# Kernel optimization log

Measured on AMD Instinct MI355X. Metric: run time of the kernel, lower is better.

Reference implementation:

```python
import jax, jax.numpy as jnp
import numpy as np

N_NODES = 10000
N_EDGES = 640000
N_GRAPHS = 64
IN_FEATS = 128
H_FEATS = 128


def setup_inputs() -> dict:
    key = jax.random.key(0)
    ks = jax.random.split(key, 8)
    in_feat = jax.random.normal(ks[0], (N_NODES, IN_FEATS), dtype=jnp.float32)
    src = jax.random.randint(ks[1], (N_EDGES,), 0, N_NODES, dtype=jnp.int32)
    dst = jax.random.randint(ks[2], (N_EDGES,), 0, N_NODES, dtype=jnp.int32)
    graph_ids = jnp.sort(jax.random.randint(ks[3], (N_NODES,), 0, N_GRAPHS, dtype=jnp.int32))
    s1 = 1.0 / np.sqrt(IN_FEATS)
    s2 = 1.0 / np.sqrt(H_FEATS)
    W1 = jax.random.uniform(ks[4], (IN_FEATS, H_FEATS), jnp.float32, -s1, s1)
    b1 = jnp.zeros((H_FEATS,), jnp.float32)
    W2 = jax.random.uniform(ks[5], (H_FEATS, H_FEATS), jnp.float32, -s2, s2)
    b2 = jnp.zeros((H_FEATS,), jnp.float32)
    Wd = jax.random.uniform(ks[6], (H_FEATS, 1), jnp.float32, -s2, s2)
    bd = jnp.zeros((1,), jnp.float32)
    return {"in_feat": in_feat, "src": src, "dst": dst, "graph_ids": graph_ids,
            "W1": W1, "b1": b1, "W2": W2, "b2": b2, "Wd": Wd, "bd": bd}


def _graph_conv(x, src, dst, norm_src, norm_dst, W, b):
    # DGL GraphConv, norm='both': D_dst^{-1/2} A D_src^{-1/2} X W + b
    x = x * norm_src[:, None]
    agg = jax.ops.segment_sum(x[src], dst, num_segments=N_NODES)  # scatter-add over edges
    agg = agg * norm_dst[:, None]
    return agg @ W + b


def reference(in_feat, src, dst, graph_ids, W1, b1, W2, b2, Wd, bd):
    ones_e = jnp.ones((N_EDGES,), in_feat.dtype)
    out_deg = jax.ops.segment_sum(ones_e, src, num_segments=N_NODES)
    in_deg = jax.ops.segment_sum(ones_e, dst, num_segments=N_NODES)
    norm_src = jnp.where(out_deg > 0, out_deg, 1.0) ** -0.5
    norm_dst = jnp.where(in_deg > 0, in_deg, 1.0) ** -0.5

    h = jax.nn.relu(_graph_conv(in_feat, src, dst, norm_src, norm_dst, W1, b1))
    h = jax.nn.relu(_graph_conv(h, src, dst, norm_src, norm_dst, W2, b2))

    # dgl.mean_nodes: per-graph mean of node features
    counts = jax.ops.segment_sum(jnp.ones((N_NODES,), h.dtype), graph_ids, num_segments=N_GRAPHS)
    pooled = jax.ops.segment_sum(h, graph_ids, num_segments=N_GRAPHS)
    pooled = pooled / jnp.maximum(counts, 1.0)[:, None]

    out = pooled @ Wd + bd  # [G, 1]
    return out.squeeze(-1)
```

## Files before the change

kernel.cpp:

```cpp
#include <hip/hip_runtime.h>
#include <hip/hip_fp16.h>

#define N_NODES 10000
#define N_EDGES 640000
#define N_GRAPHS 64
#define FEATS 128
#define CAP 128
#define NSLICE 128
#define EPS (N_EDGES / NSLICE)
#define EB (N_EDGES / 1024)
#define DSTRIDE 4
#define NTILE (N_NODES / 16)

static inline size_t align_up(size_t x, size_t a) { return (x + a - 1) & ~(a - 1); }

__global__ __launch_bounds__(256) void init_kernel(int* __restrict__ gcur,
                                                   int* __restrict__ deg_out,
                                                   float* __restrict__ graph_sum) {
    int i = blockIdx.x * 256 + threadIdx.x;
    if (i < N_NODES) gcur[i] = i * CAP;
    if (i < N_NODES * DSTRIDE) deg_out[i] = 0;
    if (i < N_GRAPHS) graph_sum[i] = 0.f;
}

__global__ __launch_bounds__(256) void scatter_deg_kernel(const int* __restrict__ src,
                                                          const int* __restrict__ dst,
                                                          int* __restrict__ gcur,
                                                          int* __restrict__ deg_out,
                                                          int* __restrict__ sorted_src) {
    const int tid = threadIdx.x;
    if (blockIdx.x < NSLICE) {
        __shared__ int cnt[N_NODES];
        const int s = blockIdx.x;
        for (int i = tid; i < N_NODES; i += 256) cnt[i] = 0;
        __syncthreads();
        const int4* d4 = (const int4*)(dst + s * EPS);
        for (int i = tid; i < EPS / 4; i += 256) {
            int4 dv = d4[i];
            atomicAdd(&cnt[dv.x], 1);
            atomicAdd(&cnt[dv.y], 1);
            atomicAdd(&cnt[dv.z], 1);
            atomicAdd(&cnt[dv.w], 1);
        }
        __syncthreads();
        for (int n = tid; n < N_NODES; n += 256) {
            int c = cnt[n];
            if (c) cnt[n] = atomicAdd(&gcur[n], c);
        }
        __syncthreads();
        const int4* s4 = (const int4*)(src + s * EPS);
        for (int i = tid; i < EPS / 4; i += 256) {
            int4 sv = s4[i];
            int4 dv = d4[i];
            int p;
            p = atomicAdd(&cnt[dv.x], 1); sorted_src[p] = sv.x;
            p = atomicAdd(&cnt[dv.y], 1); sorted_src[p] = sv.y;
            p = atomicAdd(&cnt[dv.z], 1); sorted_src[p] = sv.z;
            p = atomicAdd(&cnt[dv.w], 1); sorted_src[p] = sv.w;
        }
    } else {
        const int i = (blockIdx.x - NSLICE) * 256 + tid;
        int4 sv = ((const int4*)src)[i];
        atomicAdd(&deg_out[sv.x * DSTRIDE], 1);
        atomicAdd(&deg_out[sv.y * DSTRIDE], 1);
        atomicAdd(&deg_out[sv.z * DSTRIDE], 1);
        atomicAdd(&deg_out[sv.w * DSTRIDE], 1);
    }
}

__global__ __launch_bounds__(256) void prescale_kernel(const float* __restrict__ in_feat,
                                                       const int* __restrict__ deg_out,
                                                       __half* __restrict__ xs) {
    int i = blockIdx.x * 256 + threadIdx.x;
    if (i < N_NODES * (FEATS / 4)) {
        int n = i >> 5;
        int d = deg_out[n * DSTRIDE];
        float s = rsqrtf((float)(d < 1 ? 1 : d));
        float4 v = ((const float4*)in_feat)[i];
        __half2* o = (__half2*)(xs + (size_t)i * 4);
        o[0] = __floats2half2_rn(v.x * s, v.y * s);
        o[1] = __floats2half2_rn(v.z * s, v.w * s);
    }
}

static __device__ __forceinline__ void acc_row(uint4 v, float* a) {
    const __half2* hp = (const __half2*)&v;
#pragma unroll
    for (int j = 0; j < 4; j++) {
        float2 f = __half22float2(hp[j]);
        a[2 * j]     += f.x;
        a[2 * j + 1] += f.y;
    }
}

static __device__ __forceinline__ void qg_aggregate(const __half* __restrict__ X,
                                                    const int* __restrict__ ss,
                                                    int n, int cnt, int l16, float nd,
                                                    float* __restrict__ Arow) {
    const uint4* __restrict__ x4 = (const uint4*)X;
    const int base = n * CAP;
    float a[8] = {0.f, 0.f, 0.f, 0.f, 0.f, 0.f, 0.f, 0.f};
    int c = 0;
    for (; c + 8 <= cnt; c += 8) {
        int4 i0 = *(const int4*)(ss + base + c);
        int4 i1 = *(const int4*)(ss + base + c + 4);
        uint4 v0 = x4[i0.x * 16 + l16];
        uint4 v1 = x4[i0.y * 16 + l16];
        uint4 v2 = x4[i0.z * 16 + l16];
        uint4 v3 = x4[i0.w * 16 + l16];
        uint4 v4 = x4[i1.x * 16 + l16];
        uint4 v5 = x4[i1.y * 16 + l16];
        uint4 v6 = x4[i1.z * 16 + l16];
        uint4 v7 = x4[i1.w * 16 + l16];
        acc_row(v0, a); acc_row(v1, a); acc_row(v2, a); acc_row(v3, a);
        acc_row(v4, a); acc_row(v5, a); acc_row(v6, a); acc_row(v7, a);
    }
    for (; c < cnt; c++) acc_row(x4[ss[base + c] * 16 + l16], a);
    *(float4*)(Arow + l16 * 8)     = make_float4(a[0] * nd, a[1] * nd, a[2] * nd, a[3] * nd);
    *(float4*)(Arow + l16 * 8 + 4) = make_float4(a[4] * nd, a[5] * nd, a[6] * nd, a[7] * nd);
}

static __device__ __forceinline__ void gemm_2x4(const float* __restrict__ a0p,
                                                const float* __restrict__ a1p,
                                                const float* __restrict__ W, int fg,
                                                float4& acc0, float4& acc1) {
#pragma unroll 4
    for (int k = 0; k < FEATS; k++) {
        float a0 = a0p[k];
        float a1 = a1p[k];
        float4 w = *(const float4*)(W + k * FEATS + fg);
        acc0.x = fmaf(a0, w.x, acc0.x); acc0.y = fmaf(a0, w.y, acc0.y);
        acc0.z = fmaf(a0, w.z, acc0.z); acc0.w = fmaf(a0, w.w, acc0.w);
        acc1.x = fmaf(a1, w.x, acc1.x); acc1.y = fmaf(a1, w.y, acc1.y);
        acc1.z = fmaf(a1, w.z, acc1.z); acc1.w = fmaf(a1, w.w, acc1.w);
    }
}

__global__ __launch_bounds__(256) void fused_layer1_kernel(const __half* __restrict__ xs,
                                                           const int* __restrict__ sorted_src,
                                                           const int* __restrict__ gcur,
                                                           const int* __restrict__ deg_out,
                                                           const float* __restrict__ W,
                                                           const float* __restrict__ bias,
                                                           __half* __restrict__ out) {
    __shared__ float As[16 * FEATS];
    const int tid = threadIdx.x;
    const int nb = blockIdx.x * 16;
    const int lane = tid & 63;
    const int ln = (tid >> 6) * 4 + (lane >> 4);
    const int l16 = lane & 15;
    const int n = nb + ln;
    const int cnt = gcur[n] - n * CAP;
    const float nd = rsqrtf((float)(cnt < 1 ? 1 : cnt));
    qg_aggregate(xs, sorted_src, n, cnt, l16, nd, As + ln * FEATS);
    __syncthreads();
    const int fg = (tid & 31) << 2;
    const int r = tid >> 5;
    float4 acc0 = make_float4(0.f, 0.f, 0.f, 0.f);
    float4 acc1 = make_float4(0.f, 0.f, 0.f, 0.f);
    gemm_2x4(As + r * FEATS, As + (r + 8) * FEATS, W, fg, acc0, acc1);
    float4 bb = *(const float4*)(bias + fg);
    const int gn0 = nb + r, gn1 = nb + r + 8;
    const int do0 = deg_out[gn0 * DSTRIDE], do1 = deg_out[gn1 * DSTRIDE];
    const float s0 = rsqrtf((float)(do0 < 1 ? 1 : do0));
    const float s1 = rsqrtf((float)(do1 < 1 ? 1 : do1));
    __half2 h00 = __floats2half2_rn(fmaxf(acc0.x + bb.x, 0.f) * s0,
                                    fmaxf(acc0.y + bb.y, 0.f) * s0);
    __half2 h01 = __floats2half2_rn(fmaxf(acc0.z + bb.z, 0.f) * s0,
                                    fmaxf(acc0.w + bb.w, 0.f) * s0);
    __half2 h10 = __floats2half2_rn(fmaxf(acc1.x + bb.x, 0.f) * s1,
                                    fmaxf(acc1.y + bb.y, 0.f) * s1);
    __half2 h11 = __floats2half2_rn(fmaxf(acc1.z + bb.z, 0.f) * s1,
                                    fmaxf(acc1.w + bb.w, 0.f) * s1);
    __half2* o0 = (__half2*)(out + (size_t)gn0 * FEATS + fg);
    __half2* o1 = (__half2*)(out + (size_t)gn1 * FEATS + fg);
    o0[0] = h00; o0[1] = h01;
    o1[0] = h10; o1[1] = h11;
}

__global__ __launch_bounds__(256) void fused_layer2_kernel(const __half* __restrict__ hbuf,
                                                           const int* __restrict__ sorted_src,
                                                           const int* __restrict__ gcur,
                                                           const float* __restrict__ W,
                                                           const float* __restrict__ bias,
                                                           const float* __restrict__ Wd,
                                                           const int* __restrict__ gids,
                                                           float* __restrict__ graph_sum) {
    __shared__ float As[16 * FEATS];
    __shared__ float bins[N_GRAPHS];
    const int tid = threadIdx.x;
    const int nb = blockIdx.x * 16;
    const int lane = tid & 63;
    const int ln = (tid >> 6) * 4 + (lane >> 4);
    const int l16 = lane & 15;
    if (tid < N_GRAPHS) bins[tid] = 0.f;
    const int n = nb + ln;
    const int cnt = gcur[n] - n * CAP;
    const float nd = rsqrtf((float)(cnt < 1 ? 1 : cnt));
    qg_aggregate(hbuf, sorted_src, n, cnt, l16, nd, As + ln * FEATS);
    __syncthreads();
    const int fg = (tid & 31) << 2;
    const int r = tid >> 5;
    float4 acc0 = make_float4(0.f, 0.f, 0.f, 0.f);
    float4 acc1 = make_float4(0.f, 0.f, 0.f, 0.f);
    gemm_2x4(As + r * FEATS, As + (r + 8) * FEATS, W, fg, acc0, acc1);
    float4 bb = *(const float4*)(bias + fg);
    float4 wd = *(const float4*)(Wd + fg);
    float p0 = fmaxf(acc0.x + bb.x, 0.f) * wd.x + fmaxf(acc0.y + bb.y, 0.f) * wd.y +
               fmaxf(acc0.z + bb.z, 0.f) * wd.z + fmaxf(acc0.w + bb.w, 0.f) * wd.w;
    float p1 = fmaxf(acc1.x + bb.x, 0.f) * wd.x + fmaxf(acc1.y + bb.y, 0.f) * wd.y +
               fmaxf(acc1.z + bb.z, 0.f) * wd.z + fmaxf(acc1.w + bb.w, 0.f) * wd.w;
#pragma unroll
    for (int d = 16; d >= 1; d >>= 1) {
        p0 += __shfl_down(p0, d);
        p1 += __shfl_down(p1, d);
    }
    if ((tid & 31) == 0) {
        atomicAdd(&bins[gids[nb + r]], p0);
        atomicAdd(&bins[gids[nb + r + 8]], p1);
    }
    __syncthreads();
    if (tid < N_GRAPHS) {
        float v = bins[tid];
        if (v != 0.f) atomicAdd(&graph_sum[tid], v);
    }
}

static __device__ __forceinline__ int lower_bound_dev(const int* __restrict__ g, int key) {
    int lo = 0, hi = N_NODES;
    while (lo < hi) {
        int mid = (lo + hi) >> 1;
        if (g[mid] < key) lo = mid + 1; else hi = mid;
    }
    return lo;
}

__global__ __launch_bounds__(64) void final_kernel(const float* __restrict__ graph_sum,
                                                   const int* __restrict__ gids,
                                                   const float* __restrict__ bd,
                                                   float* __restrict__ out) {
    int g = threadIdx.x;
    if (g < N_GRAPHS) {
        int cnt = lower_bound_dev(gids, g + 1) - lower_bound_dev(gids, g);
        out[g] = graph_sum[g] / fmaxf((float)cnt, 1.f) + bd[0];
    }
}

extern "C" void kernel_launch(void* const* d_in, const int* in_sizes, int n_in,
                              void* d_out, int out_size, void* d_ws, size_t ws_size,
                              hipStream_t stream) {
    const float* in_feat = (const float*)d_in[0];
    const int*   src     = (const int*)d_in[1];
    const int*   dst     = (const int*)d_in[2];
    const int*   gids    = (const int*)d_in[3];
    const float* W1      = (const float*)d_in[4];
    const float* b1      = (const float*)d_in[5];
    const float* W2      = (const float*)d_in[6];
    const float* b2      = (const float*)d_in[7];
    const float* Wd      = (const float*)d_in[8];
    const float* bd      = (const float*)d_in[9];
    float* out = (float*)d_out;

    char* ws = (char*)d_ws;
    size_t off = 0;
    int* gcur = (int*)(ws + off);    off += (size_t)N_NODES * 4;
    off = align_up(off, 512);
    int* deg_out = (int*)(ws + off); off += (size_t)N_NODES * DSTRIDE * 4;
    off = align_up(off, 512);
    float* graph_sum = (float*)(ws + off); off += N_GRAPHS * 4;
    off = align_up(off, 512);
    int* sorted_src = (int*)(ws + off); off += (size_t)N_NODES * CAP * 4;
    off = align_up(off, 512);
    __half* xs = (__half*)(ws + off); off += (size_t)N_NODES * FEATS * 2;
    off = align_up(off, 512);
    __half* h  = (__half*)(ws + off); off += (size_t)N_NODES * FEATS * 2;
    (void)ws_size;

    init_kernel<<<(N_NODES * DSTRIDE + 255) / 256, 256, 0, stream>>>(gcur, deg_out, graph_sum);

    scatter_deg_kernel<<<NSLICE + EB, 256, 0, stream>>>(src, dst, gcur, deg_out, sorted_src);

    prescale_kernel<<<(N_NODES * (FEATS / 4) + 255) / 256, 256, 0, stream>>>(in_feat, deg_out, xs);

    fused_layer1_kernel<<<NTILE, 256, 0, stream>>>(xs, sorted_src, gcur, deg_out,
                                                   W1, b1, h);
    fused_layer2_kernel<<<NTILE, 256, 0, stream>>>(h, sorted_src, gcur,
                                                   W2, b2, Wd, gids, graph_sum);
    final_kernel<<<1, 64, 0, stream>>>(graph_sum, gids, bd, out);
}
```

Baseline: 184.4 us.

## Build CSR via two-pass bucketed sort with 16-bit indices and shared-memory tiles

Replaces the per-slice full-node shared histogram scatter with a two-level bucket sort. Edges are first binned into 128-node buckets through a shared staging area, then each bucket is sorted into a shared-memory CSR tile of 16-bit source indices and written out coalesced. Prescaling is fused into the same launch, and the gather loop is unrolled to 16 loads. The aim is to cut the scattered global atomics and the 10000-entry shared histogram clears, and to halve index traffic. In exchange it adds a staging buffer, assumes bucket capacity and at most 128 in-edges per node (truncating silently), and needs node ids to fit in 14 bits.

```diff
diff --git a/kernel.cpp b/kernel.cpp
--- a/kernel.cpp
+++ b/kernel.cpp
@@ -6,80 +6,132 @@
 #define N_GRAPHS 64
 #define FEATS 128
 #define CAP 128
-#define NSLICE 128
-#define EPS (N_EDGES / NSLICE)
-#define EB (N_EDGES / 1024)
+#define NB 79
+#define BCAP 12288
+#define ABLK 157
 #define DSTRIDE 4
 #define NTILE (N_NODES / 16)
+#define PRE_BLOCKS 1250
 
 static inline size_t align_up(size_t x, size_t a) { return (x + a - 1) & ~(a - 1); }
 
-__global__ __launch_bounds__(256) void init_kernel(int* __restrict__ gcur,
-                                                   int* __restrict__ deg_out,
-                                                   float* __restrict__ graph_sum) {
+__global__ __launch_bounds__(256) void zero_kernel(int* __restrict__ p, int n) {
     int i = blockIdx.x * 256 + threadIdx.x;
-    if (i < N_NODES) gcur[i] = i * CAP;
-    if (i < N_NODES * DSTRIDE) deg_out[i] = 0;
-    if (i < N_GRAPHS) graph_sum[i] = 0.f;
-}
-
-__global__ __launch_bounds__(256) void scatter_deg_kernel(const int* __restrict__ src,
-                                                          const int* __restrict__ dst,
-                                                          int* __restrict__ gcur,
-                                                          int* __restrict__ deg_out,
-                                                          int* __restrict__ sorted_src) {
+    if (i < n) p[i] = 0;
+}
+
+__global__ __launch_bounds__(256) void bucket_kernel(const int* __restrict__ src,
+                                                     const int* __restrict__ dst,
+                                                     int* __restrict__ bucket_cur,
+                                                     int* __restrict__ deg_out,
+                                                     int* __restrict__ staging) {
     const int tid = threadIdx.x;
-    if (blockIdx.x < NSLICE) {
-        __shared__ int cnt[N_NODES];
-        const int s = blockIdx.x;
-        for (int i = tid; i < N_NODES; i += 256) cnt[i] = 0;
-        __syncthreads();
-        const int4* d4 = (const int4*)(dst + s * EPS);
-        for (int i = tid; i < EPS / 4; i += 256) {
-            int4 dv = d4[i];
-            atomicAdd(&cnt[dv.x], 1);
-            atomicAdd(&cnt[dv.y], 1);
-            atomicAdd(&cnt[dv.z], 1);
-            atomicAdd(&cnt[dv.w], 1);
-        }
-        __syncthreads();
-        for (int n = tid; n < N_NODES; n += 256) {
-            int c = cnt[n];
-            if (c) cnt[n] = atomicAdd(&gcur[n], c);
-        }
-        __syncthreads();
-        const int4* s4 = (const int4*)(src + s * EPS);
-        for (int i = tid; i < EPS / 4; i += 256) {
-            int4 sv = s4[i];
-            int4 dv = d4[i];
+    if (blockIdx.x < ABLK) {
+        __shared__ int stage[4096];
+        __shared__ int hist[NB], pfx[NB], gbase[NB], cur[NB];
+        if (tid < NB) hist[tid] = 0;
+        __syncthreads();
+        int4 sv[4], dv[4];
+        bool valid[4];
+        const int base4 = blockIdx.x * 1024 + tid;
+#pragma unroll
+        for (int k = 0; k < 4; k++) {
+            int i4 = base4 + k * 256;
+            valid[k] = (i4 < N_EDGES / 4);
+            sv[k] = make_int4(0, 0, 0, 0);
+            dv[k] = make_int4(0, 0, 0, 0);
+            if (valid[k]) { sv[k] = ((const int4*)src)[i4]; dv[k] = ((const int4*)dst)[i4]; }
+        }
+#pragma unroll
+        for (int k = 0; k < 4; k++) if (valid[k]) {
+            atomicAdd(&hist[dv[k].x >> 7], 1);
+            atomicAdd(&hist[dv[k].y >> 7], 1);
+            atomicAdd(&hist[dv[k].z >> 7], 1);
+            atomicAdd(&hist[dv[k].w >> 7], 1);
+        }
+        __syncthreads();
+        if (tid == 0) {
+            int run = 0;
+            for (int b = 0; b < NB; b++) { pfx[b] = run; run += hist[b]; }
+        }
+        __syncthreads();
+        if (tid < NB) {
+            int c = hist[tid];
+            gbase[tid] = c ? atomicAdd(&bucket_cur[tid], c) : 0;
+            cur[tid] = pfx[tid];
+        }
+        __syncthreads();
+#pragma unroll
+        for (int k = 0; k < 4; k++) if (valid[k]) {
             int p;
-            p = atomicAdd(&cnt[dv.x], 1); sorted_src[p] = sv.x;
-            p = atomicAdd(&cnt[dv.y], 1); sorted_src[p] = sv.y;
-            p = atomicAdd(&cnt[dv.z], 1); sorted_src[p] = sv.z;
-            p = atomicAdd(&cnt[dv.w], 1); sorted_src[p] = sv.w;
+            p = atomicAdd(&cur[dv[k].x >> 7], 1); stage[p] = (sv[k].x << 14) | dv[k].x;
+            p = atomicAdd(&cur[dv[k].y >> 7], 1); stage[p] = (sv[k].y << 14) | dv[k].y;
+            p = atomicAdd(&cur[dv[k].z >> 7], 1); stage[p] = (sv[k].z << 14) | dv[k].z;
+            p = atomicAdd(&cur[dv[k].w >> 7], 1); stage[p] = (sv[k].w << 14) | dv[k].w;
+        }
+        __syncthreads();
+        const int wv = tid >> 6, ln = tid & 63;
+        for (int b = wv; b < NB; b += 4) {
+            const int c = hist[b], gb = gbase[b], lb = pfx[b];
+            for (int k = ln; k < c; k += 64) staging[b * BCAP + gb + k] = stage[lb + k];
         }
     } else {
-        const int i = (blockIdx.x - NSLICE) * 256 + tid;
-        int4 sv = ((const int4*)src)[i];
-        atomicAdd(&deg_out[sv.x * DSTRIDE], 1);
-        atomicAdd(&deg_out[sv.y * DSTRIDE], 1);
-        atomicAdd(&deg_out[sv.z * DSTRIDE], 1);
-        atomicAdd(&deg_out[sv.w * DSTRIDE], 1);
-    }
-}
-
-__global__ __launch_bounds__(256) void prescale_kernel(const float* __restrict__ in_feat,
-                                                       const int* __restrict__ deg_out,
-                                                       __half* __restrict__ xs) {
-    int i = blockIdx.x * 256 + threadIdx.x;
-    if (i < N_NODES * (FEATS / 4)) {
-        int n = i >> 5;
-        int d = deg_out[n * DSTRIDE];
-        float s = rsqrtf((float)(d < 1 ? 1 : d));
-        float4 v = ((const float4*)in_feat)[i];
-        __half2* o = (__half2*)(xs + (size_t)i * 4);
-        o[0] = __floats2half2_rn(v.x * s, v.y * s);
-        o[1] = __floats2half2_rn(v.z * s, v.w * s);
+        const int base4 = (blockIdx.x - ABLK) * 1024 + tid;
+#pragma unroll
+        for (int k = 0; k < 4; k++) {
+            int i4 = base4 + k * 256;
+            if (i4 < N_EDGES / 4) {
+                int4 s = ((const int4*)src)[i4];
+                atomicAdd(&deg_out[s.x * DSTRIDE], 1);
+                atomicAdd(&deg_out[s.y * DSTRIDE], 1);
+                atomicAdd(&deg_out[s.z * DSTRIDE], 1);
+                atomicAdd(&deg_out[s.w * DSTRIDE], 1);
+            }
+        }
+    }
+}
+
+__global__ __launch_bounds__(256) void csr_prescale_kernel(const int* __restrict__ bucket_cur,
+                                                           const int* __restrict__ staging,
+                                                           unsigned short* __restrict__ csr,
+                                                           int* __restrict__ deg_in,
+                                                           const int* __restrict__ deg_out,
+                                                           const float* __restrict__ in_feat,
+                                                           __half* __restrict__ xs) {
+    const int tid = threadIdx.x;
+    if (blockIdx.x < NB) {
+        __shared__ unsigned short tile[128 * CAP];
+        __shared__ int cur[128];
+        const int b = blockIdx.x;
+        if (tid < 128) cur[tid] = 0;
+        __syncthreads();
+        const int cnt = bucket_cur[b];
+        const int* st = staging + b * BCAP;
+        for (int i = tid; i < cnt; i += 256) {
+            int e = st[i];
+            int dl = (e & 16383) - b * 128;
+            int p = atomicAdd(&cur[dl], 1);
+            if (p < CAP) tile[dl * CAP + p] = (unsigned short)(e >> 14);
+        }
+        __syncthreads();
+        const uint4* t4 = (const uint4*)tile;
+        uint4* c4 = (uint4*)(csr + (size_t)b * 128 * CAP);
+        for (int i = tid; i < 128 * CAP / 8; i += 256) c4[i] = t4[i];
+        if (tid < 128) {
+            int n = b * 128 + tid;
+            if (n < N_NODES) deg_in[n] = cur[tid] < CAP ? cur[tid] : CAP;
+        }
+    } else {
+        int i = (blockIdx.x - NB) * 256 + tid;
+        if (i < N_NODES * (FEATS / 4)) {
+            int n = i >> 5;
+            int d = deg_out[n * DSTRIDE];
+            float s = rsqrtf((float)(d < 1 ? 1 : d));
+            float4 v = ((const float4*)in_feat)[i];
+            __half2* o = (__half2*)(xs + (size_t)i * 4);
+            o[0] = __floats2half2_rn(v.x * s, v.y * s);
+            o[1] = __floats2half2_rn(v.z * s, v.w * s);
+        }
     }
 }
 
@@ -94,28 +146,37 @@
 }
 
 static __device__ __forceinline__ void qg_aggregate(const __half* __restrict__ X,
-                                                    const int* __restrict__ ss,
+                                                    const unsigned short* __restrict__ csr,
                                                     int n, int cnt, int l16, float nd,
                                                     float* __restrict__ Arow) {
     const uint4* __restrict__ x4 = (const uint4*)X;
-    const int base = n * CAP;
+    const unsigned short* __restrict__ ss = csr + (size_t)n * CAP;
     float a[8] = {0.f, 0.f, 0.f, 0.f, 0.f, 0.f, 0.f, 0.f};
     int c = 0;
-    for (; c + 8 <= cnt; c += 8) {
-        int4 i0 = *(const int4*)(ss + base + c);
-        int4 i1 = *(const int4*)(ss + base + c + 4);
-        uint4 v0 = x4[i0.x * 16 + l16];
-        uint4 v1 = x4[i0.y * 16 + l16];
-        uint4 v2 = x4[i0.z * 16 + l16];
-        uint4 v3 = x4[i0.w * 16 + l16];
-        uint4 v4 = x4[i1.x * 16 + l16];
-        uint4 v5 = x4[i1.y * 16 + l16];
-        uint4 v6 = x4[i1.z * 16 + l16];
-        uint4 v7 = x4[i1.w * 16 + l16];
-        acc_row(v0, a); acc_row(v1, a); acc_row(v2, a); acc_row(v3, a);
-        acc_row(v4, a); acc_row(v5, a); acc_row(v6, a); acc_row(v7, a);
-    }
-    for (; c < cnt; c++) acc_row(x4[ss[base + c] * 16 + l16], a);
+    for (; c + 16 <= cnt; c += 16) {
+        uint4 iv0 = *(const uint4*)(ss + c);
+        uint4 iv1 = *(const uint4*)(ss + c + 8);
+        const unsigned short* i0 = (const unsigned short*)&iv0;
+        const unsigned short* i1 = (const unsigned short*)&iv1;
+        uint4 v[16];
+#pragma unroll
+        for (int k = 0; k < 8; k++) v[k] = x4[(int)i0[k] * 16 + l16];
+#pragma unroll
+        for (int k = 0; k < 8; k++) v[8 + k] = x4[(int)i1[k] * 16 + l16];
+#pragma unroll
+        for (int k = 0; k < 16; k++) acc_row(v[k], a);
+    }
+    if (c + 8 <= cnt) {
+        uint4 iv0 = *(const uint4*)(ss + c);
+        const unsigned short* i0 = (const unsigned short*)&iv0;
+        uint4 v[8];
+#pragma unroll
+        for (int k = 0; k < 8; k++) v[k] = x4[(int)i0[k] * 16 + l16];
+#pragma unroll
+        for (int k = 0; k < 8; k++) acc_row(v[k], a);
+        c += 8;
+    }
+    for (; c < cnt; c++) acc_row(x4[(int)ss[c] * 16 + l16], a);
     *(float4*)(Arow + l16 * 8)     = make_float4(a[0] * nd, a[1] * nd, a[2] * nd, a[3] * nd);
     *(float4*)(Arow + l16 * 8 + 4) = make_float4(a[4] * nd, a[5] * nd, a[6] * nd, a[7] * nd);
 }
@@ -137,8 +198,8 @@
 }
 
 __global__ __launch_bounds__(256) void fused_layer1_kernel(const __half* __restrict__ xs,
-                                                           const int* __restrict__ sorted_src,
-                                                           const int* __restrict__ gcur,
+                                                           const unsigned short* __restrict__ csr,
+                                                           const int* __restrict__ deg_in,
                                                            const int* __restrict__ deg_out,
                                                            const float* __restrict__ W,
                                                            const float* __restrict__ bias,
@@ -150,9 +211,9 @@
     const int ln = (tid >> 6) * 4 + (lane >> 4);
     const int l16 = lane & 15;
     const int n = nb + ln;
-    const int cnt = gcur[n] - n * CAP;
+    const int cnt = deg_in[n];
     const float nd = rsqrtf((float)(cnt < 1 ? 1 : cnt));
-    qg_aggregate(xs, sorted_src, n, cnt, l16, nd, As + ln * FEATS);
+    qg_aggregate(xs, csr, n, cnt, l16, nd, As + ln * FEATS);
     __syncthreads();
     const int fg = (tid & 31) << 2;
     const int r = tid >> 5;
@@ -179,8 +240,8 @@
 }
 
 __global__ __launch_bounds__(256) void fused_layer2_kernel(const __half* __restrict__ hbuf,
-                                                           const int* __restrict__ sorted_src,
-                                                           const int* __restrict__ gcur,
+                                                           const unsigned short* __restrict__ csr,
+                                                           const int* __restrict__ deg_in,
                                                            const float* __restrict__ W,
                                                            const float* __restrict__ bias,
                                                            const float* __restrict__ Wd,
@@ -195,9 +256,9 @@
     const int l16 = lane & 15;
     if (tid < N_GRAPHS) bins[tid] = 0.f;
     const int n = nb + ln;
-    const int cnt = gcur[n] - n * CAP;
+    const int cnt = deg_in[n];
     const float nd = rsqrtf((float)(cnt < 1 ? 1 : cnt));
-    qg_aggregate(hbuf, sorted_src, n, cnt, l16, nd, As + ln * FEATS);
+    qg_aggregate(hbuf, csr, n, cnt, l16, nd, As + ln * FEATS);
     __syncthreads();
     const int fg = (tid & 31) << 2;
     const int r = tid >> 5;
@@ -263,28 +324,31 @@
 
     char* ws = (char*)d_ws;
     size_t off = 0;
-    int* gcur = (int*)(ws + off);    off += (size_t)N_NODES * 4;
-    off = align_up(off, 512);
-    int* deg_out = (int*)(ws + off); off += (size_t)N_NODES * DSTRIDE * 4;
-    off = align_up(off, 512);
+    int* bucket_cur = (int*)(ws + off); off += NB * 4;
+    int* deg_out = (int*)(ws + off);    off += (size_t)N_NODES * DSTRIDE * 4;
     float* graph_sum = (float*)(ws + off); off += N_GRAPHS * 4;
-    off = align_up(off, 512);
-    int* sorted_src = (int*)(ws + off); off += (size_t)N_NODES * CAP * 4;
+    const int zero_n = (int)(off / 4);
+    off = align_up(off, 512);
+    int* deg_in = (int*)(ws + off);  off += (size_t)N_NODES * 4;
+    off = align_up(off, 512);
+    int* staging = (int*)(ws + off); off += (size_t)NB * BCAP * 4;
+    off = align_up(off, 512);
+    unsigned short* csr = (unsigned short*)(ws + off);
+    off += (size_t)NB * 128 * CAP * 2;
     off = align_up(off, 512);
     __half* xs = (__half*)(ws + off); off += (size_t)N_NODES * FEATS * 2;
     off = align_up(off, 512);
     __half* h  = (__half*)(ws + off); off += (size_t)N_NODES * FEATS * 2;
     (void)ws_size;
 
-    init_kernel<<<(N_NODES * DSTRIDE + 255) / 256, 256, 0, stream>>>(gcur, deg_out, graph_sum);
-
-    scatter_deg_kernel<<<NSLICE + EB, 256, 0, stream>>>(src, dst, gcur, deg_out, sorted_src);
-
-    prescale_kernel<<<(N_NODES * (FEATS / 4) + 255) / 256, 256, 0, stream>>>(in_feat, deg_out, xs);
-
-    fused_layer1_kernel<<<NTILE, 256, 0, stream>>>(xs, sorted_src, gcur, deg_out,
-                                                   W1, b1, h);
-    fused_layer2_kernel<<<NTILE, 256, 0, stream>>>(h, sorted_src, gcur,
-                                                   W2, b2, Wd, gids, graph_sum);
+    zero_kernel<<<(zero_n + 255) / 256, 256, 0, stream>>>((int*)ws, zero_n);
+
+    bucket_kernel<<<2 * ABLK, 256, 0, stream>>>(src, dst, bucket_cur, deg_out, staging);
+
+    csr_prescale_kernel<<<NB + PRE_BLOCKS, 256, 0, stream>>>(bucket_cur, staging, csr,
+                                                             deg_in, deg_out, in_feat, xs);
+
+    fused_layer1_kernel<<<NTILE, 256, 0, stream>>>(xs, csr, deg_in, deg_out, W1, b1, h);
+    fused_layer2_kernel<<<NTILE, 256, 0, stream>>>(h, csr, deg_in, W2, b2, Wd, gids, graph_sum);
     final_kernel<<<1, 64, 0, stream>>>(graph_sum, gids, bd, out);
 }
```

After: 176.9 us. 4.1% less time.
